# Kernel tuning notes

Hardware: AMD Instinct MI355X
Metric: run time of the kernel (lower is better)

## Reference

```python
import jax, jax.numpy as jnp
import numpy as np

C = 1024      # channels
K = 7         # kernel_size
G = 1         # groups (G>1 crashes in the original torch code; see notes)
GC = C // G   # group_channels
OFFSET_SCALE = 2.0
LN_EPS = 1e-5


def setup_inputs() -> dict:
    key = jax.random.key(0)
    ks = jax.random.split(key, 8)
    N, L = 4, 2048
    s = 1.0 / np.sqrt(C)
    x = jax.random.normal(ks[0], (N, L, C), jnp.float32)
    Wi = jax.random.normal(ks[1], (C, C), jnp.float32) * s
    bi = jnp.zeros((C,), jnp.float32)
    dw_w = jax.random.normal(ks[2], (C, 1, 3), jnp.float32) * 0.5   # depthwise conv kernel (O, I/g=1, W)
    dw_b = jnp.zeros((C,), jnp.float32)
    ln_g = jnp.ones((C,), jnp.float32)
    ln_b = jnp.zeros((C,), jnp.float32)
    Wo = jax.random.normal(ks[3], (G * K, C), jnp.float32) * 0.02   # offset head (nonzero to exercise gather)
    bo = jnp.zeros((G * K,), jnp.float32)
    Wm = jax.random.normal(ks[4], (G * K, C), jnp.float32) * 0.02   # mask head
    bm = jnp.zeros((G * K,), jnp.float32)
    Wout = jax.random.normal(ks[5], (C, C), jnp.float32) * s
    bout = jnp.zeros((C,), jnp.float32)
    return {"x": x, "Wi": Wi, "bi": bi, "dw_w": dw_w, "dw_b": dw_b,
            "ln_g": ln_g, "ln_b": ln_b, "Wo": Wo, "bo": bo,
            "Wm": Wm, "bm": bm, "Wout": Wout, "bout": bout}


def _forward(x, Wi, bi, dw_w, dw_b, ln_g, ln_b, Wo, bo, Wm, bm, Wout, bout):
    N, L, Cc = x.shape
    dt = x.dtype
    # input projection
    x_proj = x @ Wi.T + bi                                  # [N,L,C]
    # depthwise conv (k=3, pad=1, groups=C) -> LayerNorm(C) -> GELU(exact)
    y = jax.lax.conv_general_dilated(
        x.transpose(0, 2, 1), dw_w, window_strides=(1,), padding=((1, 1),),
        dimension_numbers=("NCH", "OIH", "NCH"), feature_group_count=Cc)
    x_dw = y.transpose(0, 2, 1) + dw_b                       # [N,L,C]
    mu = x_dw.mean(-1, keepdims=True)
    var = ((x_dw - mu) ** 2).mean(-1, keepdims=True)
    x_dw = (x_dw - mu) * jax.lax.rsqrt(var + LN_EPS) * ln_g + ln_b
    x_dw = jax.nn.gelu(x_dw, approximate=False)
    # dynamic offsets and sampling mask
    offsets = (x_dw @ Wo.T + bo).reshape(N, L, G, K) * OFFSET_SCALE
    mask = jax.nn.softmax((x_dw @ Wm.T + bm).reshape(N, L, G, K), axis=-1)
    mask = jnp.nan_to_num(mask, nan=0.0)
    # absolute sampling positions
    ref_off = jnp.linspace(-(K // 2), K // 2, K).astype(dt)          # [K]
    pos = jnp.arange(L, dtype=dt)[None, :, None, None]               # [1,L,1,1]
    abs_pos = pos + ref_off[None, None, None, :] + offsets           # [N,L,G,K]
    apc = jnp.clip(abs_pos, 0.0, L - 1)
    p_floor = jnp.clip(apc.astype(jnp.int32), 0, L - 1)
    p_ceil = jnp.clip(p_floor + 1, 0, L - 1)
    w_ceil = apc - p_floor.astype(dt)
    w_floor = 1.0 - w_ceil
    valid = jnp.logical_not((abs_pos < 0) | (abs_pos > L - 1)).astype(dt)
    w_floor = w_floor * valid
    w_ceil = w_ceil * valid
    # gather + bilinear blend (G=1: each sample index grabs the full C channels)
    idx_f = p_floor.reshape(N, -1)[:, :, None]                       # [N, L*G*K, 1]
    idx_c = p_ceil.reshape(N, -1)[:, :, None]
    v_floor = jnp.take_along_axis(x_proj, idx_f, axis=1).reshape(N, L, G, K, GC)
    v_ceil = jnp.take_along_axis(x_proj, idx_c, axis=1).reshape(N, L, G, K, GC)
    sampled = v_floor * w_floor[..., None] + v_ceil * w_ceil[..., None]
    out = (sampled * mask[..., None]).sum(axis=3).reshape(N, L, Cc)  # sum over K
    return out @ Wout.T + bout


def reference(x, Wi, bi, dw_w, dw_b, ln_g, ln_b, Wo, bo, Wm, bm, Wout, bout):
    return _forward(x, Wi, bi, dw_w, dw_b, ln_g, ln_b, Wo, bo, Wm, bm, Wout, bout)
```

## Files before the change

### kernel.cpp

```cpp
#include <hip/hip_runtime.h>
#include <hip/hip_bf16.h>
#include <cstdint>

#define C_DIM 1024
#define L_DIM 2048
#define N_DIM 4
#define M_DIM (N_DIM * L_DIM)

typedef __attribute__((ext_vector_type(8))) short frag8;
typedef __attribute__((ext_vector_type(4))) float f32x4;

__device__ __forceinline__ void gl_lds16(const void* g, void* l) {
  __builtin_amdgcn_global_load_lds((const __attribute__((address_space(1))) void*)g,
                                   (__attribute__((address_space(3))) void*)l,
                                   16, 0, 0);
}
__device__ __forceinline__ void store_out(float* Y, size_t idx, float v) { Y[idx] = v; }
__device__ __forceinline__ void store_out(__hip_bfloat16* Y, size_t idx, float v) {
  Y[idx] = __float2bfloat16(v);
}
__device__ __forceinline__ float4 ldbf4(const __hip_bfloat16* p) {
  union { short4 s; __hip_bfloat16 h[4]; } u; u.s = *(const short4*)p;
  return make_float4((float)u.h[0], (float)u.h[1], (float)u.h[2], (float)u.h[3]);
}
__device__ __forceinline__ void stbf4(__hip_bfloat16* p, float4 v) {
  union { short4 s; __hip_bfloat16 h[4]; } u;
  u.h[0] = __float2bfloat16(v.x); u.h[1] = __float2bfloat16(v.y);
  u.h[2] = __float2bfloat16(v.z); u.h[3] = __float2bfloat16(v.w);
  *(short4*)p = u.s;
}

__global__ __launch_bounds__(256)
void cvt_f32_bf16(const float* __restrict__ in, __hip_bfloat16* __restrict__ out, int n8) {
  const int i = blockIdx.x * 256 + threadIdx.x;
  if (i >= n8) return;
  const float4 a = *(const float4*)(in + (size_t)i * 8);
  const float4 b = *(const float4*)(in + (size_t)i * 8 + 4);
  union { __hip_bfloat16 h[8]; int4 q; } u;
  u.h[0] = __float2bfloat16(a.x); u.h[1] = __float2bfloat16(a.y);
  u.h[2] = __float2bfloat16(a.z); u.h[3] = __float2bfloat16(a.w);
  u.h[4] = __float2bfloat16(b.x); u.h[5] = __float2bfloat16(b.y);
  u.h[6] = __float2bfloat16(b.z); u.h[7] = __float2bfloat16(b.w);
  *(int4*)(out + (size_t)i * 8) = u.q;
}

template <typename TY>
__global__ __launch_bounds__(256, 2)
void gemm_lds(const __hip_bfloat16* __restrict__ X,
              const __hip_bfloat16* __restrict__ W,
              const float* __restrict__ bias,
              TY* __restrict__ Y, int M, int N, int K)
{
  __shared__ __hip_bfloat16 As[128 * 32];
  __shared__ __hip_bfloat16 Bs[128 * 32];
  const int tid  = threadIdx.x;
  const int lane = tid & 63;
  const int wave = tid >> 6;
  const int bm = blockIdx.x * 128;
  const int bn = blockIdx.y * 128;
  const int wr = (wave >> 1) * 64;
  const int wc = (wave & 1) * 64;
  const int srow  = tid >> 2;
  const int skoff = (tid & 3) * 8;

  f32x4 acc[4][4] = {};
  const __hip_bfloat16* gA0 = X + (size_t)(bm + srow) * K + skoff;
  const __hip_bfloat16* gA1 = X + (size_t)(bm + 64 + srow) * K + skoff;
  const __hip_bfloat16* gB0 = W + (size_t)(bn + srow) * K + skoff;
  const __hip_bfloat16* gB1 = W + (size_t)(bn + 64 + srow) * K + skoff;

  const int arow  = lane & 15;
  const int akoff = (lane >> 4) * 8;

  for (int k0 = 0; k0 < K; k0 += 32) {
    gl_lds16(gA0 + k0, &As[tid * 8]);
    gl_lds16(gA1 + k0, &As[2048 + tid * 8]);
    gl_lds16(gB0 + k0, &Bs[tid * 8]);
    gl_lds16(gB1 + k0, &Bs[2048 + tid * 8]);
    __syncthreads();

    frag8 a[4], b[4];
#pragma unroll
    for (int i = 0; i < 4; i++)
      a[i] = *(const frag8*)&As[(wr + i * 16 + arow) * 32 + akoff];
#pragma unroll
    for (int j = 0; j < 4; j++)
      b[j] = *(const frag8*)&Bs[(wc + j * 16 + arow) * 32 + akoff];
#pragma unroll
    for (int i = 0; i < 4; i++)
#pragma unroll
      for (int j = 0; j < 4; j++)
        acc[i][j] = __builtin_amdgcn_mfma_f32_16x16x32_bf16(a[i], b[j], acc[i][j], 0, 0, 0);
    __syncthreads();
  }

#pragma unroll
  for (int i = 0; i < 4; i++)
#pragma unroll
    for (int j = 0; j < 4; j++) {
      const int col = bn + wc + j * 16 + (lane & 15);
      const float bv = bias[col];
#pragma unroll
      for (int r = 0; r < 4; r++) {
        const int row = bm + wr + i * 16 + (lane >> 4) * 4 + r;
        store_out(Y, (size_t)row * N + col, acc[i][j][r] + bv);
      }
    }
}

struct Ld8f { float4 a, b; };
struct Ld8b { int4 a; };
__device__ __forceinline__ Ld8f ld8(const float* p) {
  return { *(const float4*)p, *(const float4*)(p + 4) };
}
__device__ __forceinline__ Ld8b ld8(const __hip_bfloat16* p) { return { *(const int4*)p }; }
__device__ __forceinline__ void st8(__hip_bfloat16* l, const Ld8f& v) {
  union { __hip_bfloat16 h[8]; int4 q; } u;
  u.h[0] = __float2bfloat16(v.a.x); u.h[1] = __float2bfloat16(v.a.y);
  u.h[2] = __float2bfloat16(v.a.z); u.h[3] = __float2bfloat16(v.a.w);
  u.h[4] = __float2bfloat16(v.b.x); u.h[5] = __float2bfloat16(v.b.y);
  u.h[6] = __float2bfloat16(v.b.z); u.h[7] = __float2bfloat16(v.b.w);
  *(int4*)l = u.q;
}
__device__ __forceinline__ void st8(__hip_bfloat16* l, const Ld8b& v) { *(int4*)l = v.a; }

template <typename TX, typename TY>
__global__ __launch_bounds__(256, 2)
void gemm_nt(const TX* __restrict__ X, const float* __restrict__ W,
             const float* __restrict__ bias, TY* __restrict__ Y, int M, int N, int K)
{
  __shared__ __hip_bfloat16 As[128 * 32];
  __shared__ __hip_bfloat16 Bs[128 * 32];
  const int tid  = threadIdx.x;
  const int lane = tid & 63;
  const int wave = tid >> 6;
  const int bm = blockIdx.x * 128;
  const int bn = blockIdx.y * 128;
  const int wr = (wave >> 1) * 64;
  const int wc = (wave & 1) * 64;
  const int srow  = tid >> 2;
  const int skoff = (tid & 3) * 8;

  f32x4 acc[4][4] = {};
  const TX*    gA0 = X + (size_t)(bm + srow) * K + skoff;
  const TX*    gA1 = X + (size_t)(bm + 64 + srow) * K + skoff;
  const float* gB0 = W + (size_t)(bn + srow) * K + skoff;
  const float* gB1 = W + (size_t)(bn + 64 + srow) * K + skoff;
  const int arow  = lane & 15;
  const int akoff = (lane >> 4) * 8;

  for (int k0 = 0; k0 < K; k0 += 32) {
    const auto va0 = ld8(gA0 + k0);
    const auto va1 = ld8(gA1 + k0);
    const auto vb0 = ld8(gB0 + k0);
    const auto vb1 = ld8(gB1 + k0);
    __syncthreads();
    st8(&As[srow * 32 + skoff],        va0);
    st8(&As[(64 + srow) * 32 + skoff], va1);
    st8(&Bs[srow * 32 + skoff],        vb0);
    st8(&Bs[(64 + srow) * 32 + skoff], vb1);
    __syncthreads();

    frag8 a[4], b[4];
#pragma unroll
    for (int i = 0; i < 4; i++)
      a[i] = *(const frag8*)&As[(wr + i * 16 + arow) * 32 + akoff];
#pragma unroll
    for (int j = 0; j < 4; j++)
      b[j] = *(const frag8*)&Bs[(wc + j * 16 + arow) * 32 + akoff];
#pragma unroll
    for (int i = 0; i < 4; i++)
#pragma unroll
      for (int j = 0; j < 4; j++)
        acc[i][j] = __builtin_amdgcn_mfma_f32_16x16x32_bf16(a[i], b[j], acc[i][j], 0, 0, 0);
  }
#pragma unroll
  for (int i = 0; i < 4; i++)
#pragma unroll
    for (int j = 0; j < 4; j++) {
      const int col = bn + wc + j * 16 + (lane & 15);
      const float bv = bias[col];
#pragma unroll
      for (int r = 0; r < 4; r++) {
        const int row = bm + wr + i * 16 + (lane >> 4) * 4 + r;
        store_out(Y, (size_t)row * N + col, acc[i][j][r] + bv);
      }
    }
}

__global__ __launch_bounds__(256)
void mid_fused_v2(const float* __restrict__ x,
                  const float* __restrict__ dw_w, const float* __restrict__ dw_b,
                  const float* __restrict__ ln_g, const float* __restrict__ ln_b,
                  const float* __restrict__ Wo,   const float* __restrict__ bo,
                  const float* __restrict__ Wm,   const float* __restrict__ bmb,
                  const __hip_bfloat16* __restrict__ xp,
                  __hip_bfloat16* __restrict__ smp)
{
  const int b    = blockIdx.x;
  const int bs   = (b & 7) * 256 + (b >> 3);
  const int wid  = threadIdx.x >> 6;
  const int lane = threadIdx.x & 63;
  const int row  = bs * 4 + wid;
  const int l    = row & (L_DIM - 1);
  const int n    = row >> 11;

  const float* xr = x + (size_t)row * C_DIM;

  float4 v[4];
#pragma unroll
  for (int j = 0; j < 4; j++) {
    const int c4 = j * 256 + lane * 4;
    const float4 x0 = *(const float4*)(xr + c4);
    float4 xm = make_float4(0.f, 0.f, 0.f, 0.f);
    float4 xq = make_float4(0.f, 0.f, 0.f, 0.f);
    if (l > 0)         xm = *(const float4*)(xr + c4 - C_DIM);
    if (l < L_DIM - 1) xq = *(const float4*)(xr + c4 + C_DIM);
    const float4 w0 = *(const float4*)(dw_w + (size_t)c4 * 3);
    const float4 w1 = *(const float4*)(dw_w + (size_t)c4 * 3 + 4);
    const float4 w2 = *(const float4*)(dw_w + (size_t)c4 * 3 + 8);
    const float4 bb = *(const float4*)(dw_b + c4);
    v[j].x = xm.x * w0.x + x0.x * w0.y + xq.x * w0.z + bb.x;
    v[j].y = xm.y * w0.w + x0.y * w1.x + xq.y * w1.y + bb.y;
    v[j].z = xm.z * w1.z + x0.z * w1.w + xq.z * w2.x + bb.z;
    v[j].w = xm.w * w2.y + x0.w * w2.z + xq.w * w2.w + bb.w;
  }

  float s1 = 0.f, s2 = 0.f;
#pragma unroll
  for (int j = 0; j < 4; j++) {
    s1 += v[j].x + v[j].y + v[j].z + v[j].w;
    s2 += v[j].x * v[j].x + v[j].y * v[j].y + v[j].z * v[j].z + v[j].w * v[j].w;
  }
#pragma unroll
  for (int m = 1; m < 64; m <<= 1) { s1 += __shfl_xor(s1, m); s2 += __shfl_xor(s2, m); }
  const float mu   = s1 * (1.f / C_DIM);
  const float var  = s2 * (1.f / C_DIM) - mu * mu;
  const float rstd = rsqrtf(var + 1e-5f);

  float4 g[4];
#pragma unroll
  for (int j = 0; j < 4; j++) {
    const int c4 = j * 256 + lane * 4;
    const float4 gg = *(const float4*)(ln_g + c4);
    const float4 bb = *(const float4*)(ln_b + c4);
    float t;
    t = (v[j].x - mu) * rstd * gg.x + bb.x; g[j].x = 0.5f * t * (1.f + erff(t * 0.70710678f));
    t = (v[j].y - mu) * rstd * gg.y + bb.y; g[j].y = 0.5f * t * (1.f + erff(t * 0.70710678f));
    t = (v[j].z - mu) * rstd * gg.z + bb.z; g[j].z = 0.5f * t * (1.f + erff(t * 0.70710678f));
    t = (v[j].w - mu) * rstd * gg.w + bb.w; g[j].w = 0.5f * t * (1.f + erff(t * 0.70710678f));
  }

  float po[7] = {0,0,0,0,0,0,0}, pm[7] = {0,0,0,0,0,0,0};
#pragma unroll
  for (int k = 0; k < 7; k++) {
#pragma unroll
    for (int j = 0; j < 4; j++) {
      const int c4 = j * 256 + lane * 4;
      const float4 wo = *(const float4*)(Wo + (size_t)k * C_DIM + c4);
      const float4 wm = *(const float4*)(Wm + (size_t)k * C_DIM + c4);
      po[k] += g[j].x * wo.x + g[j].y * wo.y + g[j].z * wo.z + g[j].w * wo.w;
      pm[k] += g[j].x * wm.x + g[j].y * wm.y + g[j].z * wm.z + g[j].w * wm.w;
    }
  }
#pragma unroll
  for (int k = 0; k < 7; k++)
#pragma unroll
    for (int m = 1; m < 64; m <<= 1) {
      po[k] += __shfl_xor(po[k], m);
      pm[k] += __shfl_xor(pm[k], m);
    }

  float lg[7], mx = -1e30f;
#pragma unroll
  for (int k = 0; k < 7; k++) { lg[k] = pm[k] + bmb[k]; mx = fmaxf(mx, lg[k]); }
  float se = 0.f, e[7];
#pragma unroll
  for (int k = 0; k < 7; k++) { e[k] = __expf(lg[k] - mx); se += e[k]; }
  const float inv = 1.f / se;

  float wf[7], wcl[7]; int pf[7], pc[7];
#pragma unroll
  for (int k = 0; k < 7; k++) {
    const float msk = e[k] * inv;
    const float off = (po[k] + bo[k]) * 2.0f;
    const float ap  = (float)l + (float)(k - 3) + off;
    const float apc = fminf(fmaxf(ap, 0.f), (float)(L_DIM - 1));
    int f = (int)apc;
    int c = f + 1; if (c > L_DIM - 1) c = L_DIM - 1;
    const float w1  = apc - (float)f;
    const float val = (ap < 0.f || ap > (float)(L_DIM - 1)) ? 0.f : 1.f;
    wf[k] = (1.f - w1) * val * msk;
    wcl[k] = w1 * val * msk;
    pf[k] = f; pc[k] = c;
  }

  const __hip_bfloat16* xpn = xp + ((size_t)n * L_DIM) * C_DIM;
  __hip_bfloat16* so = smp + (size_t)row * C_DIM;
#pragma unroll
  for (int j = 0; j < 4; j++) {
    const int c4 = j * 256 + lane * 4;
    float4 a = make_float4(0.f, 0.f, 0.f, 0.f);
#pragma unroll
    for (int k = 0; k < 7; k++) {
      const float4 vf = ldbf4(xpn + (size_t)pf[k] * C_DIM + c4);
      const float4 vc = ldbf4(xpn + (size_t)pc[k] * C_DIM + c4);
      a.x += wf[k] * vf.x + wcl[k] * vc.x;
      a.y += wf[k] * vf.y + wcl[k] * vc.y;
      a.z += wf[k] * vf.z + wcl[k] * vc.z;
      a.w += wf[k] * vf.w + wcl[k] * vc.w;
    }
    stbf4(so + c4, a);
  }
}

extern "C" void kernel_launch(void* const* d_in, const int* in_sizes, int n_in,
                              void* d_out, int out_size, void* d_ws, size_t ws_size,
                              hipStream_t stream)
{
  const float* x    = (const float*)d_in[0];
  const float* Wi   = (const float*)d_in[1];
  const float* bi   = (const float*)d_in[2];
  const float* dw_w = (const float*)d_in[3];
  const float* dw_b = (const float*)d_in[4];
  const float* ln_g = (const float*)d_in[5];
  const float* ln_b = (const float*)d_in[6];
  const float* Wo   = (const float*)d_in[7];
  const float* bo   = (const float*)d_in[8];
  const float* Wm   = (const float*)d_in[9];
  const float* bm   = (const float*)d_in[10];
  const float* Wout = (const float*)d_in[11];
  const float* bout = (const float*)d_in[12];
  float* out = (float*)d_out;

  const size_t XE = (size_t)M_DIM * C_DIM;
  const size_t WE = (size_t)C_DIM * C_DIM;
  char* wsb = (char*)d_ws;
  __hip_bfloat16* xp    = (__hip_bfloat16*)wsb;
  __hip_bfloat16* smp   = (__hip_bfloat16*)(wsb + XE * 2);
  __hip_bfloat16* Wib   = (__hip_bfloat16*)(wsb + XE * 4);
  __hip_bfloat16* Woutb = (__hip_bfloat16*)(wsb + XE * 4 + WE * 2);
  __hip_bfloat16* xb    = (__hip_bfloat16*)(wsb + XE * 4 + WE * 4);

  const size_t need_w2   = XE * 4 + WE * 4;
  const size_t need_full = need_w2 + XE * 2;

  dim3 gg(M_DIM / 128, C_DIM / 128);

  if (ws_size >= need_full) {
    cvt_f32_bf16<<<(int)(XE / 8 / 256), 256, 0, stream>>>(x, xb, (int)(XE / 8));
    cvt_f32_bf16<<<(int)(WE / 8 / 256), 256, 0, stream>>>(Wi, Wib, (int)(WE / 8));
    cvt_f32_bf16<<<(int)(WE / 8 / 256), 256, 0, stream>>>(Wout, Woutb, (int)(WE / 8));
    gemm_lds<__hip_bfloat16><<<gg, 256, 0, stream>>>(xb, Wib, bi, xp, M_DIM, C_DIM, C_DIM);
    mid_fused_v2<<<M_DIM / 4, 256, 0, stream>>>(x, dw_w, dw_b, ln_g, ln_b, Wo, bo, Wm, bm, xp, smp);
    gemm_lds<float><<<gg, 256, 0, stream>>>(smp, Woutb, bout, out, M_DIM, C_DIM, C_DIM);
  } else if (ws_size >= need_w2) {
    cvt_f32_bf16<<<(int)(WE / 8 / 256), 256, 0, stream>>>(Wout, Woutb, (int)(WE / 8));
    gemm_nt<float, __hip_bfloat16><<<gg, 256, 0, stream>>>(x, Wi, bi, xp, M_DIM, C_DIM, C_DIM);
    mid_fused_v2<<<M_DIM / 4, 256, 0, stream>>>(x, dw_w, dw_b, ln_g, ln_b, Wo, bo, Wm, bm, xp, smp);
    gemm_lds<float><<<gg, 256, 0, stream>>>(smp, Woutb, bout, out, M_DIM, C_DIM, C_DIM);
  } else {
    gemm_nt<float, __hip_bfloat16><<<gg, 256, 0, stream>>>(x, Wi, bi, xp, M_DIM, C_DIM, C_DIM);
    mid_fused_v2<<<M_DIM / 4, 256, 0, stream>>>(x, dw_w, dw_b, ln_g, ln_b, Wo, bo, Wm, bm, xp, smp);
    gemm_nt<__hip_bfloat16, float><<<gg, 256, 0, stream>>>(smp, Wout, bout, out, M_DIM, C_DIM, C_DIM);
  }
}
```

Measured before the change: 213.0 us.

## Use 32x32 MFMA in GEMMs, two rows per wave, fast GELU

The LDS GEMM now uses 32x32x16 bf16 MFMA instructions with 2x2 tiles per wave instead of 4x4 tiles of 16x16x32, which cuts LDS fragment reads per MFMA. The mid kernel processes two adjacent rows per wave, sharing the depthwise-conv neighbour loads and halving the block count. Exact erf GELU is replaced by a tanh-style sigmoid approximation, which is cheaper but slightly less accurate. The mid kernel may also use more registers.

```diff
diff --git a/kernel.cpp b/kernel.cpp
--- a/kernel.cpp
+++ b/kernel.cpp
@@ -8,7 +8,8 @@
 #define M_DIM (N_DIM * L_DIM)
 
 typedef __attribute__((ext_vector_type(8))) short frag8;
-typedef __attribute__((ext_vector_type(4))) float f32x4;
+typedef __attribute__((ext_vector_type(4)))  float f32x4;
+typedef __attribute__((ext_vector_type(16))) float f32x16;
 
 __device__ __forceinline__ void gl_lds16(const void* g, void* l) {
   __builtin_amdgcn_global_load_lds((const __attribute__((address_space(1))) void*)g,
@@ -28,6 +29,11 @@
   u.h[0] = __float2bfloat16(v.x); u.h[1] = __float2bfloat16(v.y);
   u.h[2] = __float2bfloat16(v.z); u.h[3] = __float2bfloat16(v.w);
   *(short4*)p = u.s;
+}
+__device__ __forceinline__ float gelu_fast(float t) {
+  const float t3 = t * t * t;
+  const float ns = -1.5957691216f * t - 0.0713548163f * t3;
+  return t / (1.f + __expf(ns));
 }
 
 __global__ __launch_bounds__(256)
@@ -46,10 +52,10 @@
 
 template <typename TY>
 __global__ __launch_bounds__(256, 2)
-void gemm_lds(const __hip_bfloat16* __restrict__ X,
-              const __hip_bfloat16* __restrict__ W,
-              const float* __restrict__ bias,
-              TY* __restrict__ Y, int M, int N, int K)
+void gemm_lds32(const __hip_bfloat16* __restrict__ X,
+                const __hip_bfloat16* __restrict__ W,
+                const float* __restrict__ bias,
+                TY* __restrict__ Y, int M, int N, int K)
 {
   __shared__ __hip_bfloat16 As[128 * 32];
   __shared__ __hip_bfloat16 Bs[128 * 32];
@@ -63,14 +69,14 @@
   const int srow  = tid >> 2;
   const int skoff = (tid & 3) * 8;
 
-  f32x4 acc[4][4] = {};
+  f32x16 acc[2][2] = {};
   const __hip_bfloat16* gA0 = X + (size_t)(bm + srow) * K + skoff;
   const __hip_bfloat16* gA1 = X + (size_t)(bm + 64 + srow) * K + skoff;
   const __hip_bfloat16* gB0 = W + (size_t)(bn + srow) * K + skoff;
   const __hip_bfloat16* gB1 = W + (size_t)(bn + 64 + srow) * K + skoff;
 
-  const int arow  = lane & 15;
-  const int akoff = (lane >> 4) * 8;
+  const int arow  = lane & 31;
+  const int akoff = (lane >> 5) * 8;
 
   for (int k0 = 0; k0 < K; k0 += 32) {
     gl_lds16(gA0 + k0, &As[tid * 8]);
@@ -79,30 +85,33 @@
     gl_lds16(gB1 + k0, &Bs[2048 + tid * 8]);
     __syncthreads();
 
-    frag8 a[4], b[4];
-#pragma unroll
-    for (int i = 0; i < 4; i++)
-      a[i] = *(const frag8*)&As[(wr + i * 16 + arow) * 32 + akoff];
-#pragma unroll
-    for (int j = 0; j < 4; j++)
-      b[j] = *(const frag8*)&Bs[(wc + j * 16 + arow) * 32 + akoff];
-#pragma unroll
-    for (int i = 0; i < 4; i++)
-#pragma unroll
-      for (int j = 0; j < 4; j++)
-        acc[i][j] = __builtin_amdgcn_mfma_f32_16x16x32_bf16(a[i], b[j], acc[i][j], 0, 0, 0);
+    frag8 a[2][2], b[2][2];
+#pragma unroll
+    for (int i = 0; i < 2; i++)
+#pragma unroll
+      for (int h = 0; h < 2; h++) {
+        a[i][h] = *(const frag8*)&As[(wr + i * 32 + arow) * 32 + h * 16 + akoff];
+        b[i][h] = *(const frag8*)&Bs[(wc + i * 32 + arow) * 32 + h * 16 + akoff];
+      }
+#pragma unroll
+    for (int h = 0; h < 2; h++)
+#pragma unroll
+      for (int i = 0; i < 2; i++)
+#pragma unroll
+        for (int j = 0; j < 2; j++)
+          acc[i][j] = __builtin_amdgcn_mfma_f32_32x32x16_bf16(a[i][h], b[j][h], acc[i][j], 0, 0, 0);
     __syncthreads();
   }
 
 #pragma unroll
-  for (int i = 0; i < 4; i++)
-#pragma unroll
-    for (int j = 0; j < 4; j++) {
-      const int col = bn + wc + j * 16 + (lane & 15);
+  for (int i = 0; i < 2; i++)
+#pragma unroll
+    for (int j = 0; j < 2; j++) {
+      const int col = bn + wc + j * 32 + (lane & 31);
       const float bv = bias[col];
 #pragma unroll
-      for (int r = 0; r < 4; r++) {
-        const int row = bm + wr + i * 16 + (lane >> 4) * 4 + r;
+      for (int r = 0; r < 16; r++) {
+        const int row = bm + wr + i * 32 + (r & 3) + 8 * (r >> 2) + 4 * (lane >> 5);
         store_out(Y, (size_t)row * N + col, acc[i][j][r] + bv);
       }
     }
@@ -189,7 +198,7 @@
 }
 
 __global__ __launch_bounds__(256)
-void mid_fused_v2(const float* __restrict__ x,
+void mid_fused_v3(const float* __restrict__ x,
                   const float* __restrict__ dw_w, const float* __restrict__ dw_b,
                   const float* __restrict__ ln_g, const float* __restrict__ ln_b,
                   const float* __restrict__ Wo,   const float* __restrict__ bo,
@@ -198,60 +207,72 @@
                   __hip_bfloat16* __restrict__ smp)
 {
   const int b    = blockIdx.x;
-  const int bs   = (b & 7) * 256 + (b >> 3);
+  const int bs   = (b & 7) * 128 + (b >> 3);
   const int wid  = threadIdx.x >> 6;
   const int lane = threadIdx.x & 63;
-  const int row  = bs * 4 + wid;
-  const int l    = row & (L_DIM - 1);
-  const int n    = row >> 11;
-
-  const float* xr = x + (size_t)row * C_DIM;
-
-  float4 v[4];
+  const int row0 = bs * 8 + wid * 2;
+  const int l0   = row0 & (L_DIM - 1);
+  const int n    = row0 >> 11;
+
+  const float* xb = x + ((size_t)n * L_DIM) * C_DIM;
+
+  float4 v0[4], v1[4];
 #pragma unroll
   for (int j = 0; j < 4; j++) {
     const int c4 = j * 256 + lane * 4;
-    const float4 x0 = *(const float4*)(xr + c4);
-    float4 xm = make_float4(0.f, 0.f, 0.f, 0.f);
-    float4 xq = make_float4(0.f, 0.f, 0.f, 0.f);
-    if (l > 0)         xm = *(const float4*)(xr + c4 - C_DIM);
-    if (l < L_DIM - 1) xq = *(const float4*)(xr + c4 + C_DIM);
+    float4 xa = make_float4(0.f, 0.f, 0.f, 0.f);
+    float4 xd = make_float4(0.f, 0.f, 0.f, 0.f);
+    if (l0 > 0)              xa = *(const float4*)(xb + (size_t)(l0 - 1) * C_DIM + c4);
+    const float4 xm = *(const float4*)(xb + (size_t)l0 * C_DIM + c4);
+    const float4 xc = *(const float4*)(xb + (size_t)(l0 + 1) * C_DIM + c4);
+    if (l0 + 2 <= L_DIM - 1) xd = *(const float4*)(xb + (size_t)(l0 + 2) * C_DIM + c4);
     const float4 w0 = *(const float4*)(dw_w + (size_t)c4 * 3);
     const float4 w1 = *(const float4*)(dw_w + (size_t)c4 * 3 + 4);
     const float4 w2 = *(const float4*)(dw_w + (size_t)c4 * 3 + 8);
     const float4 bb = *(const float4*)(dw_b + c4);
-    v[j].x = xm.x * w0.x + x0.x * w0.y + xq.x * w0.z + bb.x;
-    v[j].y = xm.y * w0.w + x0.y * w1.x + xq.y * w1.y + bb.y;
-    v[j].z = xm.z * w1.z + x0.z * w1.w + xq.z * w2.x + bb.z;
-    v[j].w = xm.w * w2.y + x0.w * w2.z + xq.w * w2.w + bb.w;
-  }
-
-  float s1 = 0.f, s2 = 0.f;
+    v0[j].x = xa.x * w0.x + xm.x * w0.y + xc.x * w0.z + bb.x;
+    v0[j].y = xa.y * w0.w + xm.y * w1.x + xc.y * w1.y + bb.y;
+    v0[j].z = xa.z * w1.z + xm.z * w1.w + xc.z * w2.x + bb.z;
+    v0[j].w = xa.w * w2.y + xm.w * w2.z + xc.w * w2.w + bb.w;
+    v1[j].x = xm.x * w0.x + xc.x * w0.y + xd.x * w0.z + bb.x;
+    v1[j].y = xm.y * w0.w + xc.y * w1.x + xd.y * w1.y + bb.y;
+    v1[j].z = xm.z * w1.z + xc.z * w1.w + xd.z * w2.x + bb.z;
+    v1[j].w = xm.w * w2.y + xc.w * w2.z + xd.w * w2.w + bb.w;
+  }
+
+  float a1 = 0.f, a2 = 0.f, b1 = 0.f, b2 = 0.f;
 #pragma unroll
   for (int j = 0; j < 4; j++) {
-    s1 += v[j].x + v[j].y + v[j].z + v[j].w;
-    s2 += v[j].x * v[j].x + v[j].y * v[j].y + v[j].z * v[j].z + v[j].w * v[j].w;
-  }
-#pragma unroll
-  for (int m = 1; m < 64; m <<= 1) { s1 += __shfl_xor(s1, m); s2 += __shfl_xor(s2, m); }
-  const float mu   = s1 * (1.f / C_DIM);
-  const float var  = s2 * (1.f / C_DIM) - mu * mu;
-  const float rstd = rsqrtf(var + 1e-5f);
-
-  float4 g[4];
+    a1 += v0[j].x + v0[j].y + v0[j].z + v0[j].w;
+    a2 += v0[j].x * v0[j].x + v0[j].y * v0[j].y + v0[j].z * v0[j].z + v0[j].w * v0[j].w;
+    b1 += v1[j].x + v1[j].y + v1[j].z + v1[j].w;
+    b2 += v1[j].x * v1[j].x + v1[j].y * v1[j].y + v1[j].z * v1[j].z + v1[j].w * v1[j].w;
+  }
+#pragma unroll
+  for (int m = 1; m < 64; m <<= 1) {
+    a1 += __shfl_xor(a1, m); a2 += __shfl_xor(a2, m);
+    b1 += __shfl_xor(b1, m); b2 += __shfl_xor(b2, m);
+  }
+  const float mu0 = a1 * (1.f / C_DIM), mu1 = b1 * (1.f / C_DIM);
+  const float rstd0 = rsqrtf(a2 * (1.f / C_DIM) - mu0 * mu0 + 1e-5f);
+  const float rstd1 = rsqrtf(b2 * (1.f / C_DIM) - mu1 * mu1 + 1e-5f);
+
 #pragma unroll
   for (int j = 0; j < 4; j++) {
     const int c4 = j * 256 + lane * 4;
     const float4 gg = *(const float4*)(ln_g + c4);
     const float4 bb = *(const float4*)(ln_b + c4);
-    float t;
-    t = (v[j].x - mu) * rstd * gg.x + bb.x; g[j].x = 0.5f * t * (1.f + erff(t * 0.70710678f));
-    t = (v[j].y - mu) * rstd * gg.y + bb.y; g[j].y = 0.5f * t * (1.f + erff(t * 0.70710678f));
-    t = (v[j].z - mu) * rstd * gg.z + bb.z; g[j].z = 0.5f * t * (1.f + erff(t * 0.70710678f));
-    t = (v[j].w - mu) * rstd * gg.w + bb.w; g[j].w = 0.5f * t * (1.f + erff(t * 0.70710678f));
-  }
-
-  float po[7] = {0,0,0,0,0,0,0}, pm[7] = {0,0,0,0,0,0,0};
+    v0[j].x = gelu_fast((v0[j].x - mu0) * rstd0 * gg.x + bb.x);
+    v0[j].y = gelu_fast((v0[j].y - mu0) * rstd0 * gg.y + bb.y);
+    v0[j].z = gelu_fast((v0[j].z - mu0) * rstd0 * gg.z + bb.z);
+    v0[j].w = gelu_fast((v0[j].w - mu0) * rstd0 * gg.w + bb.w);
+    v1[j].x = gelu_fast((v1[j].x - mu1) * rstd1 * gg.x + bb.x);
+    v1[j].y = gelu_fast((v1[j].y - mu1) * rstd1 * gg.y + bb.y);
+    v1[j].z = gelu_fast((v1[j].z - mu1) * rstd1 * gg.z + bb.z);
+    v1[j].w = gelu_fast((v1[j].w - mu1) * rstd1 * gg.w + bb.w);
+  }
+
+  float po[2][7] = {}, pm[2][7] = {};
 #pragma unroll
   for (int k = 0; k < 7; k++) {
 #pragma unroll
@@ -259,58 +280,66 @@
       const int c4 = j * 256 + lane * 4;
       const float4 wo = *(const float4*)(Wo + (size_t)k * C_DIM + c4);
       const float4 wm = *(const float4*)(Wm + (size_t)k * C_DIM + c4);
-      po[k] += g[j].x * wo.x + g[j].y * wo.y + g[j].z * wo.z + g[j].w * wo.w;
-      pm[k] += g[j].x * wm.x + g[j].y * wm.y + g[j].z * wm.z + g[j].w * wm.w;
-    }
-  }
-#pragma unroll
-  for (int k = 0; k < 7; k++)
-#pragma unroll
-    for (int m = 1; m < 64; m <<= 1) {
-      po[k] += __shfl_xor(po[k], m);
-      pm[k] += __shfl_xor(pm[k], m);
-    }
-
-  float lg[7], mx = -1e30f;
-#pragma unroll
-  for (int k = 0; k < 7; k++) { lg[k] = pm[k] + bmb[k]; mx = fmaxf(mx, lg[k]); }
-  float se = 0.f, e[7];
-#pragma unroll
-  for (int k = 0; k < 7; k++) { e[k] = __expf(lg[k] - mx); se += e[k]; }
-  const float inv = 1.f / se;
-
-  float wf[7], wcl[7]; int pf[7], pc[7];
-#pragma unroll
-  for (int k = 0; k < 7; k++) {
-    const float msk = e[k] * inv;
-    const float off = (po[k] + bo[k]) * 2.0f;
-    const float ap  = (float)l + (float)(k - 3) + off;
-    const float apc = fminf(fmaxf(ap, 0.f), (float)(L_DIM - 1));
-    int f = (int)apc;
-    int c = f + 1; if (c > L_DIM - 1) c = L_DIM - 1;
-    const float w1  = apc - (float)f;
-    const float val = (ap < 0.f || ap > (float)(L_DIM - 1)) ? 0.f : 1.f;
-    wf[k] = (1.f - w1) * val * msk;
-    wcl[k] = w1 * val * msk;
-    pf[k] = f; pc[k] = c;
-  }
+      po[0][k] += v0[j].x * wo.x + v0[j].y * wo.y + v0[j].z * wo.z + v0[j].w * wo.w;
+      pm[0][k] += v0[j].x * wm.x + v0[j].y * wm.y + v0[j].z * wm.z + v0[j].w * wm.w;
+      po[1][k] += v1[j].x * wo.x + v1[j].y * wo.y + v1[j].z * wo.z + v1[j].w * wo.w;
+      pm[1][k] += v1[j].x * wm.x + v1[j].y * wm.y + v1[j].z * wm.z + v1[j].w * wm.w;
+    }
+  }
+#pragma unroll
+  for (int rr = 0; rr < 2; rr++)
+#pragma unroll
+    for (int k = 0; k < 7; k++)
+#pragma unroll
+      for (int m = 1; m < 64; m <<= 1) {
+        po[rr][k] += __shfl_xor(po[rr][k], m);
+        pm[rr][k] += __shfl_xor(pm[rr][k], m);
+      }
 
   const __hip_bfloat16* xpn = xp + ((size_t)n * L_DIM) * C_DIM;
-  __hip_bfloat16* so = smp + (size_t)row * C_DIM;
-#pragma unroll
-  for (int j = 0; j < 4; j++) {
-    const int c4 = j * 256 + lane * 4;
-    float4 a = make_float4(0.f, 0.f, 0.f, 0.f);
+#pragma unroll
+  for (int rr = 0; rr < 2; rr++) {
+    const int l = l0 + rr;
+    float lg[7], mx = -1e30f;
+#pragma unroll
+    for (int k = 0; k < 7; k++) { lg[k] = pm[rr][k] + bmb[k]; mx = fmaxf(mx, lg[k]); }
+    float se = 0.f, e[7];
+#pragma unroll
+    for (int k = 0; k < 7; k++) { e[k] = __expf(lg[k] - mx); se += e[k]; }
+    const float inv = 1.f / se;
+
+    float wf[7], wcl[7]; int pf[7], pc[7];
 #pragma unroll
     for (int k = 0; k < 7; k++) {
-      const float4 vf = ldbf4(xpn + (size_t)pf[k] * C_DIM + c4);
-      const float4 vc = ldbf4(xpn + (size_t)pc[k] * C_DIM + c4);
-      a.x += wf[k] * vf.x + wcl[k] * vc.x;
-      a.y += wf[k] * vf.y + wcl[k] * vc.y;
-      a.z += wf[k] * vf.z + wcl[k] * vc.z;
-      a.w += wf[k] * vf.w + wcl[k] * vc.w;
-    }
-    stbf4(so + c4, a);
+      const float msk = e[k] * inv;
+      const float off = (po[rr][k] + bo[k]) * 2.0f;
+      const float ap  = (float)l + (float)(k - 3) + off;
+      const float apc = fminf(fmaxf(ap, 0.f), (float)(L_DIM - 1));
+      int f = (int)apc;
+      int c = f + 1; if (c > L_DIM - 1) c = L_DIM - 1;
+      const float w1  = apc - (float)f;
+      const float val = (ap < 0.f || ap > (float)(L_DIM - 1)) ? 0.f : 1.f;
+      wf[k]  = (1.f - w1) * val * msk;
+      wcl[k] = w1 * val * msk;
+      pf[k] = f; pc[k] = c;
+    }
+
+    __hip_bfloat16* so = smp + (size_t)(row0 + rr) * C_DIM;
+#pragma unroll
+    for (int j = 0; j < 4; j++) {
+      const int c4 = j * 256 + lane * 4;
+      float4 acc = make_float4(0.f, 0.f, 0.f, 0.f);
+#pragma unroll
+      for (int k = 0; k < 7; k++) {
+        const float4 vf = ldbf4(xpn + (size_t)pf[k] * C_DIM + c4);
+        const float4 vc = ldbf4(xpn + (size_t)pc[k] * C_DIM + c4);
+        acc.x += wf[k] * vf.x + wcl[k] * vc.x;
+        acc.y += wf[k] * vf.y + wcl[k] * vc.y;
+        acc.z += wf[k] * vf.z + wcl[k] * vc.z;
+        acc.w += wf[k] * vf.w + wcl[k] * vc.w;
+      }
+      stbf4(so + c4, acc);
+    }
   }
 }
 
@@ -340,7 +369,7 @@
   __hip_bfloat16* smp   = (__hip_bfloat16*)(wsb + XE * 2);
   __hip_bfloat16* Wib   = (__hip_bfloat16*)(wsb + XE * 4);
   __hip_bfloat16* Woutb = (__hip_bfloat16*)(wsb + XE * 4 + WE * 2);
-  __hip_bfloat16* xb    = (__hip_bfloat16*)(wsb + XE * 4 + WE * 4);
+  __hip_bfloat16* xbb   = (__hip_bfloat16*)(wsb + XE * 4 + WE * 4);
 
   const size_t need_w2   = XE * 4 + WE * 4;
   const size_t need_full = need_w2 + XE * 2;
@@ -348,20 +377,20 @@
   dim3 gg(M_DIM / 128, C_DIM / 128);
 
   if (ws_size >= need_full) {
-    cvt_f32_bf16<<<(int)(XE / 8 / 256), 256, 0, stream>>>(x, xb, (int)(XE / 8));
+    cvt_f32_bf16<<<(int)(XE / 8 / 256), 256, 0, stream>>>(x, xbb, (int)(XE / 8));
     cvt_f32_bf16<<<(int)(WE / 8 / 256), 256, 0, stream>>>(Wi, Wib, (int)(WE / 8));
     cvt_f32_bf16<<<(int)(WE / 8 / 256), 256, 0, stream>>>(Wout, Woutb, (int)(WE / 8));
-    gemm_lds<__hip_bfloat16><<<gg, 256, 0, stream>>>(xb, Wib, bi, xp, M_DIM, C_DIM, C_DIM);
-    mid_fused_v2<<<M_DIM / 4, 256, 0, stream>>>(x, dw_w, dw_b, ln_g, ln_b, Wo, bo, Wm, bm, xp, smp);
-    gemm_lds<float><<<gg, 256, 0, stream>>>(smp, Woutb, bout, out, M_DIM, C_DIM, C_DIM);
+    gemm_lds32<__hip_bfloat16><<<gg, 256, 0, stream>>>(xbb, Wib, bi, xp, M_DIM, C_DIM, C_DIM);
+    mid_fused_v3<<<M_DIM / 8, 256, 0, stream>>>(x, dw_w, dw_b, ln_g, ln_b, Wo, bo, Wm, bm, xp, smp);
+    gemm_lds32<float><<<gg, 256, 0, stream>>>(smp, Woutb, bout, out, M_DIM, C_DIM, C_DIM);
   } else if (ws_size >= need_w2) {
     cvt_f32_bf16<<<(int)(WE / 8 / 256), 256, 0, stream>>>(Wout, Woutb, (int)(WE / 8));
     gemm_nt<float, __hip_bfloat16><<<gg, 256, 0, stream>>>(x, Wi, bi, xp, M_DIM, C_DIM, C_DIM);
-    mid_fused_v2<<<M_DIM / 4, 256, 0, stream>>>(x, dw_w, dw_b, ln_g, ln_b, Wo, bo, Wm, bm, xp, smp);
-    gemm_lds<float><<<gg, 256, 0, stream>>>(smp, Woutb, bout, out, M_DIM, C_DIM, C_DIM);
+    mid_fused_v3<<<M_DIM / 8, 256, 0, stream>>>(x, dw_w, dw_b, ln_g, ln_b, Wo, bo, Wm, bm, xp, smp);
+    gemm_lds32<float><<<gg, 256, 0, stream>>>(smp, Woutb, bout, out, M_DIM, C_DIM, C_DIM);
   } else {
     gemm_nt<float, __hip_bfloat16><<<gg, 256, 0, stream>>>(x, Wi, bi, xp, M_DIM, C_DIM, C_DIM);
-    mid_fused_v2<<<M_DIM / 4, 256, 0, stream>>>(x, dw_w, dw_b, ln_g, ln_b, Wo, bo, Wm, bm, xp, smp);
+    mid_fused_v3<<<M_DIM / 8, 256, 0, stream>>>(x, dw_w, dw_b, ln_g, ln_b, Wo, bo, Wm, bm, xp, smp);
     gemm_nt<__hip_bfloat16, float><<<gg, 256, 0, stream>>>(smp, Wout, bout, out, M_DIM, C_DIM, C_DIM);
   }
 }
```

Measured after the change: 208.8 us. 1.02x faster.
